# Kernel optimization log

Measured on AMD Instinct MI355X. Metric: run time of the kernel, lower is better.

## Reference

```python
import jax, jax.numpy as jnp
import numpy as np
import math

B, S, H, NH = 2, 2048, 2048, 16
HD = H // NH
BASE = 10000.0


def _rope_tables():
    inv_freq = 1.0 / (BASE ** (np.arange(0, HD, 2, dtype=np.float32) / HD))
    t = np.arange(S, dtype=np.float32)
    freqs = np.einsum('i,j->ij', t, inv_freq)          # [S, HD/2]
    emb = np.concatenate([freqs, freqs], axis=-1)       # [S, HD]
    return jnp.asarray(np.cos(emb)), jnp.asarray(np.sin(emb))


def setup_inputs() -> dict:
    key = jax.random.key(0)
    ks = jax.random.split(key, 6)
    scale = 1.0 / math.sqrt(H)
    cos, sin = _rope_tables()
    causal = np.triu(np.full((S, S), -1e9, dtype=np.float32), k=1)
    attn_bias = jnp.broadcast_to(jnp.asarray(causal)[None, None], (B, 1, S, S))
    return {
        'hidden_states': jax.random.normal(ks[0], (B, S, H), jnp.float32),
        'masks': jnp.zeros((B, S, S), jnp.float32),
        'attn_bias': attn_bias,
        'cos': cos,
        'sin': sin,
        'wq': jax.random.normal(ks[1], (H, H), jnp.float32) * scale,
        'wk': jax.random.normal(ks[2], (H, H), jnp.float32) * scale,
        'wv': jax.random.normal(ks[3], (H, H), jnp.float32) * scale,
        'wo': jax.random.normal(ks[4], (H, H), jnp.float32) * scale,
        'position_ids': jnp.broadcast_to(jnp.arange(S, dtype=jnp.int64)[None], (B, S)),
    }


def _rotate_half(x):
    x1, x2 = x[..., : x.shape[-1] // 2], x[..., x.shape[-1] // 2:]
    return jnp.concatenate([-x2, x1], axis=-1)


def reference(hidden_states, masks, attn_bias, cos, sin, wq, wk, wv, wo, position_ids):
    b, s, h = hidden_states.shape
    nh, hd = NH, HD
    # QKV projections (torch Linear: x @ W.T), split heads -> [b, nh, s, hd]
    def proj(w):
        return (hidden_states @ w.T).reshape(b, s, nh, hd).transpose(0, 2, 1, 3)
    q, k, v = proj(wq), proj(wk), proj(wv)
    # RoPE
    cos_p = cos[position_ids][:, None]  # [b, 1, s, hd]
    sin_p = sin[position_ids][:, None]
    q = q * cos_p + _rotate_half(q) * sin_p
    k = k * cos_p + _rotate_half(k) * sin_p
    # attention scores with additive masks (mx_attn branch, fp math)
    att = jnp.einsum('bhqd,bhkd->bhqk', q / math.sqrt(hd), k)
    att = att + attn_bias + masks[:, None]
    att = jax.nn.softmax(att, axis=-1)
    out = jnp.einsum('bhqk,bhkd->bhqd', att, v)
    out = out.transpose(0, 2, 1, 3).reshape(b, s, h)
    return out @ wo.T
```

## Files before the change

kernel.cpp:

```cpp
#include <hip/hip_runtime.h>
#include <stdint.h>

#define B_  2
#define S_  2048
#define H_  2048
#define NH_ 16
#define HD_ 128

typedef __bf16 v8bf __attribute__((ext_vector_type(8)));
typedef float  v4f  __attribute__((ext_vector_type(4)));

__device__ __forceinline__ float b2f(unsigned short u) {
  union { unsigned int i; float f; } x; x.i = ((unsigned int)u) << 16; return x.f;
}
__device__ __forceinline__ unsigned short f2b(float f) {
  union { float f; unsigned int i; } x; x.f = f;
  unsigned int r = x.i + 0x7FFFu + ((x.i >> 16) & 1u);
  return (unsigned short)(r >> 16);
}

__device__ __forceinline__ void async16(const void* g, void* l) {
  __builtin_amdgcn_global_load_lds(
      (const __attribute__((address_space(1))) void*)g,
      (__attribute__((address_space(3))) void*)l, 16, 0, 0);
}

__device__ __forceinline__ float swz_max16(float v) {
  v = fmaxf(v, __int_as_float(__builtin_amdgcn_ds_swizzle(__float_as_int(v), 0x201F)));
  v = fmaxf(v, __int_as_float(__builtin_amdgcn_ds_swizzle(__float_as_int(v), 0x101F)));
  v = fmaxf(v, __int_as_float(__builtin_amdgcn_ds_swizzle(__float_as_int(v), 0x081F)));
  v = fmaxf(v, __int_as_float(__builtin_amdgcn_ds_swizzle(__float_as_int(v), 0x041F)));
  return v;
}
__device__ __forceinline__ float swz_sum16(float v) {
  v += __int_as_float(__builtin_amdgcn_ds_swizzle(__float_as_int(v), 0x201F));
  v += __int_as_float(__builtin_amdgcn_ds_swizzle(__float_as_int(v), 0x101F));
  v += __int_as_float(__builtin_amdgcn_ds_swizzle(__float_as_int(v), 0x081F));
  v += __int_as_float(__builtin_amdgcn_ds_swizzle(__float_as_int(v), 0x041F));
  return v;
}

__global__ __launch_bounds__(256) void cvt_all(const float* __restrict__ hid,
                                               const float* __restrict__ wq,
                                               const float* __restrict__ wk,
                                               const float* __restrict__ wv,
                                               const float* __restrict__ wo,
                                               unsigned short* __restrict__ Xb,
                                               unsigned short* __restrict__ Wqb,
                                               unsigned short* __restrict__ Wkb,
                                               unsigned short* __restrict__ Wvb,
                                               unsigned short* __restrict__ Wob) {
  int bid = blockIdx.x;
  const float* src;
  unsigned short* dst;
  int rel;
  if (bid < 8192)       { src = hid; dst = Xb;  rel = bid; }
  else if (bid < 12288) { src = wq;  dst = Wqb; rel = bid - 8192; }
  else if (bid < 16384) { src = wk;  dst = Wkb; rel = bid - 12288; }
  else if (bid < 20480) { src = wv;  dst = Wvb; rel = bid - 16384; }
  else                  { src = wo;  dst = Wob; rel = bid - 20480; }
  int i = rel * 256 + threadIdx.x;
  float4 f = *(const float4*)(src + (size_t)i * 4);
  ushort4 u;
  u.x = f2b(f.x); u.y = f2b(f.y); u.z = f2b(f.z); u.w = f2b(f.w);
  *(ushort4*)(dst + (size_t)i * 4) = u;
}

__global__ __launch_bounds__(512, 2) void gemm_qkv(const unsigned short* __restrict__ X,
                                                   const unsigned short* __restrict__ Wq,
                                                   const unsigned short* __restrict__ Wk,
                                                   const unsigned short* __restrict__ Wv,
                                                   const float* __restrict__ cosT,
                                                   const float* __restrict__ sinT,
                                                   unsigned short* __restrict__ Qo,
                                                   unsigned short* __restrict__ Ko,
                                                   unsigned short* __restrict__ Vt) {
  __shared__ __align__(16) unsigned short lds[65536];
  unsigned short* ldsA = lds;
  unsigned short* ldsB = lds + 32768;

  const int tid = threadIdx.x, lane = tid & 63, w = tid >> 6;
  const int lr = lane & 15, lg = lane >> 4;
  const int wm = w >> 1, wn = w & 1;
  const int m0 = blockIdx.x * 256;
  const int by = blockIdx.y;
  const int xsw = ((lr >> 1) & 3) << 3;

  {
    const int nq = by & 7;
    const int n0 = nq * 256;
    const unsigned short* Bw = (by < 8) ? Wq : Wk;

    v4f acc[4][8];
#pragma unroll
    for (int i = 0; i < 4; i++)
#pragma unroll
      for (int j = 0; j < 8; j++) { v4f z = {0.f, 0.f, 0.f, 0.f}; acc[i][j] = z; }

    auto stage1 = [&](int ss) {
      unsigned short* Ad = ldsA + (ss & 3) * 8192;
      unsigned short* Bd = ldsB + (ss & 3) * 8192;
      const int k0 = ss * 32;
#pragma unroll
      for (int i = 0; i < 2; ++i) {
        int cbase = i * 512 + w * 64;
        int cc = cbase + lane;
        int row = cc >> 2, pos = (cc & 3) ^ ((row >> 1) & 3);
        async16(X  + (size_t)(m0 + row) * H_ + k0 + pos * 8, (char*)Ad + (size_t)cbase * 16);
        async16(Bw + (size_t)(n0 + row) * H_ + k0 + pos * 8, (char*)Bd + (size_t)cbase * 16);
      }
    };

    stage1(0); stage1(1); stage1(2);

#define QKV_SLICE(S, VMSTR) do {                                               \
    asm volatile("s_waitcnt vmcnt(" VMSTR ") lgkmcnt(0)" ::: "memory");        \
    __builtin_amdgcn_s_barrier();                                              \
    if ((S) + 3 < 64) stage1((S) + 3);                                         \
    const unsigned short* As_ = ldsA + ((S) & 3) * 8192;                       \
    const unsigned short* Bs_ = ldsB + ((S) & 3) * 8192;                       \
    v8bf bf[8], af[4];                                                         \
    _Pragma("unroll") for (int ni = 0; ni < 8; ni++)                           \
      bf[ni] = *(const v8bf*)(Bs_ + (wn * 128 + ni * 16 + lr) * 32 +           \
                              ((lg * 8) ^ xsw));                               \
    _Pragma("unroll") for (int mi = 0; mi < 4; mi++)                           \
      af[mi] = *(const v8bf*)(As_ + (wm * 64 + mi * 16 + lr) * 32 +            \
                              ((lg * 8) ^ xsw));                               \
    __builtin_amdgcn_s_setprio(1);                                             \
    _Pragma("unroll") for (int mi = 0; mi < 4; mi++)                           \
      _Pragma("unroll") for (int ni = 0; ni < 8; ni++)                         \
        acc[mi][ni] = __builtin_amdgcn_mfma_f32_16x16x32_bf16(af[mi], bf[ni],  \
                                                              acc[mi][ni], 0, 0, 0); \
    __builtin_amdgcn_s_setprio(0);                                             \
  } while (0)

    for (int s = 0; s < 62; ++s) QKV_SLICE(s, "8");
    QKV_SLICE(62, "4");
    QKV_SLICE(63, "0");
#undef QKV_SLICE

    const int h = nq * 2 + wn;
    const int rb0 = m0 + wm * 64;
    unsigned short* Out = (by < 8) ? Qo : Ko;
    const float sc = (by < 8) ? (float)(0.08838834764831845 * 1.4426950408889634) : 1.0f;
#pragma unroll
    for (int mi = 0; mi < 4; mi++)
#pragma unroll
      for (int ni = 0; ni < 4; ni++)
#pragma unroll
        for (int r = 0; r < 4; r++) {
          int row = rb0 + mi * 16 + lg * 4 + r;
          int s = row & 2047;
          int d = ni * 16 + lr;
          float c  = cosT[(size_t)s * HD_ + d];
          float sn = sinT[(size_t)s * HD_ + d];
          float x1 = acc[mi][ni][r], x2 = acc[mi][ni + 4][r];
          Out[(size_t)row * H_ + h * HD_ + d]      = f2b((x1 * c - x2 * sn) * sc);
          Out[(size_t)row * H_ + h * HD_ + d + 64] = f2b((x2 * c + x1 * sn) * sc);
        }
  }

  __syncthreads();

  {
    const int n0v = by * 128;

    v4f acc[4][4];
#pragma unroll
    for (int i = 0; i < 4; i++)
#pragma unroll
      for (int j = 0; j < 4; j++) { v4f z = {0.f, 0.f, 0.f, 0.f}; acc[i][j] = z; }

    auto stage2 = [&](int ss) {
      unsigned short* Ad = ldsA + (ss & 3) * 8192;
      unsigned short* Bd = ldsB + (ss & 3) * 4096;
      const int k0 = ss * 32;
#pragma unroll
      for (int i = 0; i < 2; ++i) {
        int cbase = i * 512 + w * 64;
        int cc = cbase + lane;
        int row = cc >> 2, pos = (cc & 3) ^ ((row >> 1) & 3);
        async16(X + (size_t)(m0 + row) * H_ + k0 + pos * 8, (char*)Ad + (size_t)cbase * 16);
      }
      {
        int cbase = w * 64;
        int cc = cbase + lane;
        int row = cc >> 2, pos = (cc & 3) ^ ((row >> 1) & 3);
        async16(Wv + (size_t)(n0v + row) * H_ + k0 + pos * 8, (char*)Bd + (size_t)cbase * 16);
      }
    };

    stage2(0); stage2(1); stage2(2);

#define V_SLICE(S, VMSTR) do {                                                 \
    asm volatile("s_waitcnt vmcnt(" VMSTR ") lgkmcnt(0)" ::: "memory");        \
    __builtin_amdgcn_s_barrier();                                              \
    if ((S) + 3 < 64) stage2((S) + 3);                                         \
    const unsigned short* As_ = ldsA + ((S) & 3) * 8192;                       \
    const unsigned short* Bs_ = ldsB + ((S) & 3) * 4096;                       \
    v8bf bf[4], af[4];                                                         \
    _Pragma("unroll") for (int ni = 0; ni < 4; ni++)                           \
      bf[ni] = *(const v8bf*)(Bs_ + (wn * 64 + ni * 16 + lr) * 32 +            \
                              ((lg * 8) ^ xsw));                               \
    _Pragma("unroll") for (int mi = 0; mi < 4; mi++)                           \
      af[mi] = *(const v8bf*)(As_ + (wm * 64 + mi * 16 + lr) * 32 +            \
                              ((lg * 8) ^ xsw));                               \
    __builtin_amdgcn_s_setprio(1);                                             \
    _Pragma("unroll") for (int mi = 0; mi < 4; mi++)                           \
      _Pragma("unroll") for (int ni = 0; ni < 4; ni++)                         \
        acc[mi][ni] = __builtin_amdgcn_mfma_f32_16x16x32_bf16(af[mi], bf[ni],  \
                                                              acc[mi][ni], 0, 0, 0); \
    __builtin_amdgcn_s_setprio(0);                                             \
  } while (0)

    for (int s = 0; s < 62; ++s) V_SLICE(s, "6");
    V_SLICE(62, "3");
    V_SLICE(63, "0");
#undef V_SLICE

    const int h = by;
#pragma unroll
    for (int mi = 0; mi < 4; mi++)
#pragma unroll
      for (int ni = 0; ni < 4; ni++) {
        int row0 = m0 + wm * 64 + mi * 16 + lg * 4;
        int b = row0 >> 11, s0 = row0 & 2047;
        int d = wn * 64 + ni * 16 + lr;
        ushort4 u;
        u.x = f2b(acc[mi][ni][0]); u.y = f2b(acc[mi][ni][1]);
        u.z = f2b(acc[mi][ni][2]); u.w = f2b(acc[mi][ni][3]);
        *(ushort4*)(Vt + ((size_t)((b * NH_ + h) * HD_) + d) * S_ + s0) = u;
      }
  }
}

__global__ __launch_bounds__(256, 2) void gemm_out(const unsigned short* __restrict__ A,
                                                   const unsigned short* __restrict__ Wo,
                                                   float* __restrict__ Out) {
  __shared__ __align__(16) unsigned short lds[32768];
  unsigned short* ldsA = lds;
  unsigned short* ldsB = lds + 16384;

  const int tid = threadIdx.x, lane = tid & 63, w = tid >> 6;
  const int lr = lane & 15, lg = lane >> 4;
  const int m0 = blockIdx.x * 128;
  const int n0 = blockIdx.y * 128;
  const int xsw = ((lr >> 1) & 3) << 3;

  v4f acc[2][8];
#pragma unroll
  for (int i = 0; i < 2; i++)
#pragma unroll
    for (int j = 0; j < 8; j++) { v4f z = {0.f, 0.f, 0.f, 0.f}; acc[i][j] = z; }

  auto stage = [&](int ss) {
    unsigned short* Ad = ldsA + (ss & 3) * 4096;
    unsigned short* Bd = ldsB + (ss & 3) * 4096;
    const int k0 = ss * 32;
#pragma unroll
    for (int i = 0; i < 2; ++i) {
      int cbase = i * 256 + w * 64;
      int cc = cbase + lane;
      int row = cc >> 2, pos = (cc & 3) ^ ((row >> 1) & 3);
      async16(A  + (size_t)(m0 + row) * H_ + k0 + pos * 8, (char*)Ad + (size_t)cbase * 16);
      async16(Wo + (size_t)(n0 + row) * H_ + k0 + pos * 8, (char*)Bd + (size_t)cbase * 16);
    }
  };

  stage(0); stage(1); stage(2);

#define O_SLICE(S, VMSTR) do {                                                 \
    asm volatile("s_waitcnt vmcnt(" VMSTR ") lgkmcnt(0)" ::: "memory");        \
    __builtin_amdgcn_s_barrier();                                              \
    if ((S) + 3 < 64) stage((S) + 3);                                          \
    const unsigned short* As_ = ldsA + ((S) & 3) * 4096;                       \
    const unsigned short* Bs_ = ldsB + ((S) & 3) * 4096;                       \
    v8bf bf[8], af[2];                                                         \
    _Pragma("unroll") for (int ni = 0; ni < 8; ni++)                           \
      bf[ni] = *(const v8bf*)(Bs_ + (ni * 16 + lr) * 32 + ((lg * 8) ^ xsw));   \
    _Pragma("unroll") for (int mi = 0; mi < 2; mi++)                           \
      af[mi] = *(const v8bf*)(As_ + (w * 32 + mi * 16 + lr) * 32 +             \
                              ((lg * 8) ^ xsw));                               \
    __builtin_amdgcn_s_setprio(1);                                             \
    _Pragma("unroll") for (int mi = 0; mi < 2; mi++)                           \
      _Pragma("unroll") for (int ni = 0; ni < 8; ni++)                         \
        acc[mi][ni] = __builtin_amdgcn_mfma_f32_16x16x32_bf16(af[mi], bf[ni],  \
                                                              acc[mi][ni], 0, 0, 0); \
    __builtin_amdgcn_s_setprio(0);                                             \
  } while (0)

  for (int s = 0; s < 62; ++s) O_SLICE(s, "8");
  O_SLICE(62, "4");
  O_SLICE(63, "0");
#undef O_SLICE

#pragma unroll
  for (int mi = 0; mi < 2; mi++)
#pragma unroll
    for (int ni = 0; ni < 8; ni++)
#pragma unroll
      for (int r = 0; r < 4; r++)
        Out[(size_t)(m0 + w * 32 + mi * 16 + lg * 4 + r) * H_ + n0 + ni * 16 + lr] =
            acc[mi][ni][r];
}

#define KT_ 64

__global__ __launch_bounds__(512, 2) void attn_kernel(const unsigned short* __restrict__ Qb,
                                                      const unsigned short* __restrict__ Kb,
                                                      const unsigned short* __restrict__ Vt,
                                                      unsigned short* __restrict__ Ob) {
  __shared__ __align__(16) char smem[83968];
  unsigned short* Ps = (unsigned short*)(smem + 65536);

  const int tid = threadIdx.x, lane = tid & 63, w = tid >> 6;
  const int lr = lane & 15, lg = lane >> 4;
  const int qp = blockIdx.x, h = blockIdx.y, b = blockIdx.z;

  const int lrow = (15 - qp) * 128 + w * 16;
  const int srow = qp * 128 + w * 16;
  const int nkt = (16 - qp) * 2;
  const int xsw = (lr & 7) << 3;

  auto stage = [&](int kt, char* Kd) {
    const int k0 = kt * KT_;
    char* Vd = Kd + 16384;
#pragma unroll
    for (int i = 0; i < 2; ++i) {
      int cbase = i * 512 + w * 64;
      int cc = cbase + lane;
      int row = cc >> 4, pos = cc & 15;
      async16(Kb + (size_t)(b * S_ + k0 + row) * H_ + h * HD_ + ((pos ^ (row & 7)) << 3),
              Kd + (size_t)cbase * 16);
    }
#pragma unroll
    for (int i = 0; i < 2; ++i) {
      int cbase = i * 512 + w * 64;
      int cc = cbase + lane;
      int row = cc >> 3, pos = cc & 7;
      async16(Vt + ((size_t)((b * NH_ + h) * HD_ + row)) * S_ + k0 + ((pos ^ (row & 7)) << 3),
              Vd + (size_t)cbase * 16);
    }
  };

  v8bf qf[2][4];
#pragma unroll
  for (int ks = 0; ks < 4; ks++) {
    qf[0][ks] = *(const v8bf*)(Qb + (size_t)(b * S_ + lrow + lr) * H_ +
                               h * HD_ + ks * 32 + lg * 8);
    qf[1][ks] = *(const v8bf*)(Qb + (size_t)(b * S_ + srow + lr) * H_ +
                               h * HD_ + ks * 32 + lg * 8);
  }

  v4f o[2][8];
#pragma unroll
  for (int mt = 0; mt < 2; mt++)
#pragma unroll
    for (int nt = 0; nt < 8; nt++) { v4f z = {0.f, 0.f, 0.f, 0.f}; o[mt][nt] = z; }
  float mst[2][4], lst[2][4];
#pragma unroll
  for (int mt = 0; mt < 2; mt++)
#pragma unroll
    for (int r = 0; r < 4; r++) { mst[mt][r] = -1e30f; lst[mt][r] = 0.f; }

  stage(0, smem);
  __syncthreads();

  int cur = 0;
  for (int kt = 0; kt < nkt; kt++) {
    char* curb = smem + cur * 32768;
    if (kt + 1 < nkt) stage(kt + 1, smem + (cur ^ 1) * 32768);

    unsigned short* Ks = (unsigned short*)curb;
    unsigned short* Vs = (unsigned short*)(curb + 16384);
    const int k0 = kt * KT_;

    if (k0 <= lrow + 15) {
      const bool act1 = (k0 <= srow + 15);
      v4f sacc[2][4];
#pragma unroll
      for (int mt = 0; mt < 2; mt++)
#pragma unroll
        for (int nt = 0; nt < 4; nt++) { v4f z = {0.f, 0.f, 0.f, 0.f}; sacc[mt][nt] = z; }
#pragma unroll
      for (int nt = 0; nt < 4; nt++) {
        v8bf kf[4];
#pragma unroll
        for (int ks = 0; ks < 4; ks++)
          kf[ks] = *(const v8bf*)(Ks + (nt * 16 + lr) * 128 + ((ks * 32 + lg * 8) ^ xsw));
#pragma unroll
        for (int ks = 0; ks < 4; ks++)
          sacc[0][nt] = __builtin_amdgcn_mfma_f32_16x16x32_bf16(qf[0][ks], kf[ks], sacc[0][nt], 0, 0, 0);
        if (act1)
#pragma unroll
          for (int ks = 0; ks < 4; ks++)
            sacc[1][nt] = __builtin_amdgcn_mfma_f32_16x16x32_bf16(qf[1][ks], kf[ks], sacc[1][nt], 0, 0, 0);
      }
      if (k0 + 63 > lrow) {
#pragma unroll
        for (int nt = 0; nt < 4; nt++)
#pragma unroll
          for (int r = 0; r < 4; r++) {
            int key = k0 + nt * 16 + lr;
            if (key > lrow + lg * 4 + r) sacc[0][nt][r] = -1e30f;
          }
      }
      if (act1 && k0 + 63 > srow) {
#pragma unroll
        for (int nt = 0; nt < 4; nt++)
#pragma unroll
          for (int r = 0; r < 4; r++) {
            int key = k0 + nt * 16 + lr;
            if (key > srow + lg * 4 + r) sacc[1][nt][r] = -1e30f;
          }
      }
#pragma unroll
      for (int mt = 0; mt < 2; mt++) {
        if (mt == 1 && !act1) continue;
        float alpha[4], rsum[4];
#pragma unroll
        for (int r = 0; r < 4; r++) {
          float v = fmaxf(fmaxf(sacc[mt][0][r], sacc[mt][1][r]),
                          fmaxf(sacc[mt][2][r], sacc[mt][3][r]));
          v = swz_max16(v);
          float mnew = fmaxf(mst[mt][r], v);
          alpha[r] = exp2f(mst[mt][r] - mnew);
          mst[mt][r] = mnew;
          rsum[r] = 0.f;
        }
#pragma unroll
        for (int nt = 0; nt < 4; nt++)
#pragma unroll
          for (int r = 0; r < 4; r++) {
            float p = exp2f(sacc[mt][nt][r] - mst[mt][r]);
            sacc[mt][nt][r] = p;
            rsum[r] += p;
          }
#pragma unroll
        for (int r = 0; r < 4; r++) {
          rsum[r] = swz_sum16(rsum[r]);
          lst[mt][r] = lst[mt][r] * alpha[r] + rsum[r];
        }
#pragma unroll
        for (int nt = 0; nt < 8; nt++)
#pragma unroll
          for (int r = 0; r < 4; r++) o[mt][nt][r] *= alpha[r];
      }
      v8bf bv[8][2];
#pragma unroll
      for (int nt = 0; nt < 8; nt++)
#pragma unroll
        for (int ks = 0; ks < 2; ks++)
          bv[nt][ks] = *(const v8bf*)(Vs + (nt * 16 + lr) * 64 + ((ks * 32 + lg * 8) ^ xsw));
#pragma unroll
      for (int mt = 0; mt < 2; mt++) {
        if (mt == 1 && !act1) continue;
#pragma unroll
        for (int nt = 0; nt < 4; nt++)
#pragma unroll
          for (int r = 0; r < 4; r++) {
            union { float f; unsigned u; } pu; pu.f = sacc[mt][nt][r];
            Ps[w * 1152 + (lg * 4 + r) * 72 + nt * 16 + lr] =
                (unsigned short)(pu.u >> 16);
          }
        asm volatile("" ::: "memory");
        v8bf af[2];
#pragma unroll
        for (int ks = 0; ks < 2; ks++)
          af[ks] = *(const v8bf*)(Ps + w * 1152 + lr * 72 + ks * 32 + lg * 8);
#pragma unroll
        for (int nt = 0; nt < 8; nt++)
#pragma unroll
          for (int ks = 0; ks < 2; ks++)
            o[mt][nt] = __builtin_amdgcn_mfma_f32_16x16x32_bf16(af[ks], bv[nt][ks], o[mt][nt], 0, 0, 0);
        asm volatile("" ::: "memory");
      }
    }
    __syncthreads();
    cur ^= 1;
  }
#pragma unroll
  for (int mt = 0; mt < 2; mt++) {
    const int rbase = (mt == 0) ? lrow : srow;
    float inv[4];
#pragma unroll
    for (int r = 0; r < 4; r++) inv[r] = 1.f / lst[mt][r];
#pragma unroll
    for (int nt = 0; nt < 8; nt++)
#pragma unroll
      for (int r = 0; r < 4; r++) {
        int row = rbase + lg * 4 + r;
        int col = h * HD_ + nt * 16 + lr;
        Ob[(size_t)(b * S_ + row) * H_ + col] = f2b(o[mt][nt][r] * inv[r]);
      }
  }
}

extern "C" void kernel_launch(void* const* d_in, const int* in_sizes, int n_in,
                              void* d_out, int out_size, void* d_ws, size_t ws_size,
                              hipStream_t stream) {
  const float* hidden = (const float*)d_in[0];
  const float* cosT = (const float*)d_in[3];
  const float* sinT = (const float*)d_in[4];
  const float* wq = (const float*)d_in[5];
  const float* wk = (const float*)d_in[6];
  const float* wv = (const float*)d_in[7];
  const float* wo = (const float*)d_in[8];
  float* out = (float*)d_out;

  char* p = (char*)d_ws;
  const size_t SZ_X = (size_t)4096 * 2048 * 2;
  const size_t SZ_W = (size_t)2048 * 2048 * 2;
  unsigned short* Xb  = (unsigned short*)p; p += SZ_X;
  unsigned short* Wqb = (unsigned short*)p; p += SZ_W;
  unsigned short* Wkb = (unsigned short*)p; p += SZ_W;
  unsigned short* Wvb = (unsigned short*)p; p += SZ_W;
  unsigned short* Wob = (unsigned short*)p; p += SZ_W;
  unsigned short* Qb  = (unsigned short*)p; p += SZ_X;
  unsigned short* Kb  = (unsigned short*)p; p += SZ_X;
  unsigned short* Vt  = (unsigned short*)p; p += SZ_X;
  unsigned short* Ob  = (unsigned short*)p; p += SZ_X;

  cvt_all<<<24576, 256, 0, stream>>>(hidden, wq, wk, wv, wo, Xb, Wqb, Wkb, Wvb, Wob);
  gemm_qkv<<<dim3(16, 16), 512, 0, stream>>>(Xb, Wqb, Wkb, Wvb, cosT, sinT, Qb, Kb, Vt);
  attn_kernel<<<dim3(8, 16, 2), 512, 0, stream>>>(Qb, Kb, Vt, Ob);
  gemm_out<<<dim3(32, 16), 256, 0, stream>>>(Ob, Wob, out);
}
```

Baseline: 402.7 us.

## Transpose QK^T MFMA so each lane owns a query row, add lazy rescale

Swaps the MFMA operands in the score product so each lane holds one query row across keys. Row max and sum then reduce mostly in registers plus two cross-lane shuffles, instead of four ds_swizzle steps per row element. Online-softmax rescaling of O is skipped unless the new max exceeds the running max by more than 8 (in log2 units), which keeps exponent growth bounded. P is stored to LDS as packed ushort4 with round-to-nearest, and s_setprio is raised around the MFMA blocks. The lazy threshold and the extra shuffles to broadcast alpha and l per output row add some complexity and numerical risk.

```diff
diff --git a/kernel.cpp b/kernel.cpp
--- a/kernel.cpp
+++ b/kernel.cpp
@@ -23,21 +23,6 @@
   __builtin_amdgcn_global_load_lds(
       (const __attribute__((address_space(1))) void*)g,
       (__attribute__((address_space(3))) void*)l, 16, 0, 0);
-}
-
-__device__ __forceinline__ float swz_max16(float v) {
-  v = fmaxf(v, __int_as_float(__builtin_amdgcn_ds_swizzle(__float_as_int(v), 0x201F)));
-  v = fmaxf(v, __int_as_float(__builtin_amdgcn_ds_swizzle(__float_as_int(v), 0x101F)));
-  v = fmaxf(v, __int_as_float(__builtin_amdgcn_ds_swizzle(__float_as_int(v), 0x081F)));
-  v = fmaxf(v, __int_as_float(__builtin_amdgcn_ds_swizzle(__float_as_int(v), 0x041F)));
-  return v;
-}
-__device__ __forceinline__ float swz_sum16(float v) {
-  v += __int_as_float(__builtin_amdgcn_ds_swizzle(__float_as_int(v), 0x201F));
-  v += __int_as_float(__builtin_amdgcn_ds_swizzle(__float_as_int(v), 0x101F));
-  v += __int_as_float(__builtin_amdgcn_ds_swizzle(__float_as_int(v), 0x081F));
-  v += __int_as_float(__builtin_amdgcn_ds_swizzle(__float_as_int(v), 0x041F));
-  return v;
 }
 
 __global__ __launch_bounds__(256) void cvt_all(const float* __restrict__ hid,
@@ -357,11 +342,9 @@
   for (int mt = 0; mt < 2; mt++)
 #pragma unroll
     for (int nt = 0; nt < 8; nt++) { v4f z = {0.f, 0.f, 0.f, 0.f}; o[mt][nt] = z; }
-  float mst[2][4], lst[2][4];
-#pragma unroll
-  for (int mt = 0; mt < 2; mt++)
-#pragma unroll
-    for (int r = 0; r < 4; r++) { mst[mt][r] = -1e30f; lst[mt][r] = 0.f; }
+  float mst[2], lst[2];
+  mst[0] = mst[1] = -1e30f;
+  lst[0] = lst[1] = 0.f;
 
   stage(0, smem);
   __syncthreads();
@@ -382,6 +365,7 @@
       for (int mt = 0; mt < 2; mt++)
 #pragma unroll
         for (int nt = 0; nt < 4; nt++) { v4f z = {0.f, 0.f, 0.f, 0.f}; sacc[mt][nt] = z; }
+      __builtin_amdgcn_s_setprio(1);
 #pragma unroll
       for (int nt = 0; nt < 4; nt++) {
         v8bf kf[4];
@@ -390,19 +374,20 @@
           kf[ks] = *(const v8bf*)(Ks + (nt * 16 + lr) * 128 + ((ks * 32 + lg * 8) ^ xsw));
 #pragma unroll
         for (int ks = 0; ks < 4; ks++)
-          sacc[0][nt] = __builtin_amdgcn_mfma_f32_16x16x32_bf16(qf[0][ks], kf[ks], sacc[0][nt], 0, 0, 0);
+          sacc[0][nt] = __builtin_amdgcn_mfma_f32_16x16x32_bf16(kf[ks], qf[0][ks], sacc[0][nt], 0, 0, 0);
         if (act1)
 #pragma unroll
           for (int ks = 0; ks < 4; ks++)
-            sacc[1][nt] = __builtin_amdgcn_mfma_f32_16x16x32_bf16(qf[1][ks], kf[ks], sacc[1][nt], 0, 0, 0);
-      }
+            sacc[1][nt] = __builtin_amdgcn_mfma_f32_16x16x32_bf16(kf[ks], qf[1][ks], sacc[1][nt], 0, 0, 0);
+      }
+      __builtin_amdgcn_s_setprio(0);
       if (k0 + 63 > lrow) {
 #pragma unroll
         for (int nt = 0; nt < 4; nt++)
 #pragma unroll
           for (int r = 0; r < 4; r++) {
-            int key = k0 + nt * 16 + lr;
-            if (key > lrow + lg * 4 + r) sacc[0][nt][r] = -1e30f;
+            int key = k0 + nt * 16 + lg * 4 + r;
+            if (key > lrow + lr) sacc[0][nt][r] = -1e30f;
           }
       }
       if (act1 && k0 + 63 > srow) {
@@ -410,41 +395,45 @@
         for (int nt = 0; nt < 4; nt++)
 #pragma unroll
           for (int r = 0; r < 4; r++) {
-            int key = k0 + nt * 16 + lr;
-            if (key > srow + lg * 4 + r) sacc[1][nt][r] = -1e30f;
+            int key = k0 + nt * 16 + lg * 4 + r;
+            if (key > srow + lr) sacc[1][nt][r] = -1e30f;
           }
       }
 #pragma unroll
       for (int mt = 0; mt < 2; mt++) {
         if (mt == 1 && !act1) continue;
-        float alpha[4], rsum[4];
-#pragma unroll
-        for (int r = 0; r < 4; r++) {
-          float v = fmaxf(fmaxf(sacc[mt][0][r], sacc[mt][1][r]),
-                          fmaxf(sacc[mt][2][r], sacc[mt][3][r]));
-          v = swz_max16(v);
-          float mnew = fmaxf(mst[mt][r], v);
-          alpha[r] = exp2f(mst[mt][r] - mnew);
-          mst[mt][r] = mnew;
-          rsum[r] = 0.f;
+        float ml = sacc[mt][0][0];
+#pragma unroll
+        for (int nt = 0; nt < 4; nt++)
+#pragma unroll
+          for (int r = 0; r < 4; r++) ml = fmaxf(ml, sacc[mt][nt][r]);
+        ml = fmaxf(ml, __shfl_xor(ml, 16, 64));
+        ml = fmaxf(ml, __shfl_xor(ml, 32, 64));
+        if (!__all(ml <= mst[mt] + 8.f)) {
+          float mnew = fmaxf(mst[mt], ml);
+          float alpha = exp2f(mst[mt] - mnew);
+          mst[mt] = mnew;
+          lst[mt] *= alpha;
+#pragma unroll
+          for (int r = 0; r < 4; r++) {
+            float a4 = __shfl(alpha, (lane & 48) | (lg * 4 + r), 64);
+#pragma unroll
+            for (int nt = 0; nt < 8; nt++) o[mt][nt][r] *= a4;
+          }
         }
+        float mm = mst[mt];
+        float rs = 0.f;
 #pragma unroll
         for (int nt = 0; nt < 4; nt++)
 #pragma unroll
           for (int r = 0; r < 4; r++) {
-            float p = exp2f(sacc[mt][nt][r] - mst[mt][r]);
+            float p = exp2f(sacc[mt][nt][r] - mm);
             sacc[mt][nt][r] = p;
-            rsum[r] += p;
+            rs += p;
           }
-#pragma unroll
-        for (int r = 0; r < 4; r++) {
-          rsum[r] = swz_sum16(rsum[r]);
-          lst[mt][r] = lst[mt][r] * alpha[r] + rsum[r];
-        }
-#pragma unroll
-        for (int nt = 0; nt < 8; nt++)
-#pragma unroll
-          for (int r = 0; r < 4; r++) o[mt][nt][r] *= alpha[r];
+        rs += __shfl_xor(rs, 16, 64);
+        rs += __shfl_xor(rs, 32, 64);
+        lst[mt] += rs;
       }
       v8bf bv[8][2];
 #pragma unroll
@@ -456,23 +445,24 @@
       for (int mt = 0; mt < 2; mt++) {
         if (mt == 1 && !act1) continue;
 #pragma unroll
-        for (int nt = 0; nt < 4; nt++)
-#pragma unroll
-          for (int r = 0; r < 4; r++) {
-            union { float f; unsigned u; } pu; pu.f = sacc[mt][nt][r];
-            Ps[w * 1152 + (lg * 4 + r) * 72 + nt * 16 + lr] =
-                (unsigned short)(pu.u >> 16);
-          }
+        for (int nt = 0; nt < 4; nt++) {
+          ushort4 u;
+          u.x = f2b(sacc[mt][nt][0]); u.y = f2b(sacc[mt][nt][1]);
+          u.z = f2b(sacc[mt][nt][2]); u.w = f2b(sacc[mt][nt][3]);
+          *(ushort4*)(Ps + w * 1152 + lr * 72 + nt * 16 + lg * 4) = u;
+        }
         asm volatile("" ::: "memory");
         v8bf af[2];
 #pragma unroll
         for (int ks = 0; ks < 2; ks++)
           af[ks] = *(const v8bf*)(Ps + w * 1152 + lr * 72 + ks * 32 + lg * 8);
+        __builtin_amdgcn_s_setprio(1);
 #pragma unroll
         for (int nt = 0; nt < 8; nt++)
 #pragma unroll
           for (int ks = 0; ks < 2; ks++)
             o[mt][nt] = __builtin_amdgcn_mfma_f32_16x16x32_bf16(af[ks], bv[nt][ks], o[mt][nt], 0, 0, 0);
+        __builtin_amdgcn_s_setprio(0);
         asm volatile("" ::: "memory");
       }
     }
@@ -484,7 +474,10 @@
     const int rbase = (mt == 0) ? lrow : srow;
     float inv[4];
 #pragma unroll
-    for (int r = 0; r < 4; r++) inv[r] = 1.f / lst[mt][r];
+    for (int r = 0; r < 4; r++) {
+      float l4 = __shfl(lst[mt], (lane & 48) | (lg * 4 + r), 64);
+      inv[r] = 1.f / l4;
+    }
 #pragma unroll
     for (int nt = 0; nt < 8; nt++)
 #pragma unroll
```

Measured after the change: 403.6 us. No clear change (+0.2%).
